# Kernel optimization log

Measured on AMD Instinct MI355X. Metric: run time of the kernel, lower is better.

Reference implementation:

```python
import jax, jax.numpy as jnp
import numpy as np

DIM, HEADS, WS, SHIFT = 192, 6, 8, 4
HEAD_DIM = DIM // HEADS
SCALE = HEAD_DIM ** -0.5
EPS = 1e-5


def _rel_pos_index(ws):
    coords = np.stack(np.meshgrid(np.arange(ws), np.arange(ws), indexing='ij'))  # [2,ws,ws]
    flat = coords.reshape(2, -1)
    rel = flat[:, :, None] - flat[:, None, :]          # [2,N,N]
    rel = rel.transpose(1, 2, 0)
    rel[:, :, 0] += ws - 1
    rel[:, :, 1] += ws - 1
    rel[:, :, 0] *= 2 * ws - 1
    return rel.sum(-1)                                  # [N,N] int


def _attn_mask(H, W, ws, shift):
    if shift == 0:
        return None
    img = np.zeros((H, W), dtype=np.float32)
    cnt = 0
    for hs in (slice(0, -ws), slice(-ws, -shift), slice(-shift, None)):
        for wsl in (slice(0, -ws), slice(-ws, -shift), slice(-shift, None)):
            img[hs, wsl] = cnt
            cnt += 1
    mw = img.reshape(H // ws, ws, W // ws, ws).transpose(0, 2, 1, 3).reshape(-1, ws * ws)  # [nW,N]
    m = mw[:, None, :] - mw[:, :, None]
    return jnp.asarray(np.where(m != 0, -100.0, 0.0).astype(np.float32))  # [nW,N,N]


def _ln(x, w, b):
    mu = x.mean(-1, keepdims=True)
    var = ((x - mu) ** 2).mean(-1, keepdims=True)
    return (x - mu) * jax.lax.rsqrt(var + EPS) * w + b


def setup_inputs() -> dict:
    key = jax.random.key(0)
    ks = jax.random.split(key, 10)
    B, H, W, C = 64, 56, 56, DIM
    hid = 4 * C
    p = lambda k, sh, s=0.02: jax.random.normal(k, sh, jnp.float32) * s
    return {
        'x': jax.random.normal(ks[0], (B, H * W, C), jnp.float32),
        'ln1_w': jnp.ones((C,), jnp.float32), 'ln1_b': jnp.zeros((C,), jnp.float32),
        'qkv_w': p(ks[1], (C, 3 * C)), 'qkv_b': jnp.zeros((3 * C,), jnp.float32),
        'proj_w': p(ks[2], (C, C)), 'proj_b': jnp.zeros((C,), jnp.float32),
        'rpb_table': p(ks[3], ((2 * WS - 1) ** 2, HEADS)),
        'ln2_w': jnp.ones((C,), jnp.float32), 'ln2_b': jnp.zeros((C,), jnp.float32),
        'fc1_w': p(ks[4], (C, hid)), 'fc1_b': jnp.zeros((hid,), jnp.float32),
        'fc2_w': p(ks[5], (hid, C)), 'fc2_b': jnp.zeros((C,), jnp.float32),
        'H': H, 'W': W,
    }


def reference(x, ln1_w, ln1_b, qkv_w, qkv_b, proj_w, proj_b, rpb_table,
              ln2_w, ln2_b, fc1_w, fc1_b, fc2_w, fc2_b, H, W):
    B, L, C = x.shape
    N = WS * WS
    shortcut = x
    xn = _ln(x, ln1_w, ln1_b).reshape(B, H, W, C)
    xn = jnp.roll(xn, (-SHIFT, -SHIFT), (1, 2))
    # window partition -> [B*nW, N, C]
    xw = xn.reshape(B, H // WS, WS, W // WS, WS, C).transpose(0, 1, 3, 2, 4, 5)
    xw = xw.reshape(-1, N, C)
    B_ = xw.shape[0]
    qkv = (xw @ qkv_w + qkv_b).reshape(B_, N, 3, HEADS, HEAD_DIM).transpose(2, 0, 3, 1, 4)
    q, k, v = qkv[0], qkv[1], qkv[2]                    # [B_,h,N,d]
    attn = jnp.einsum('bhnd,bhmd->bhnm', q * SCALE, k)
    bias = rpb_table[_rel_pos_index(WS).reshape(-1)].reshape(N, N, HEADS).transpose(2, 0, 1)
    attn = attn + bias[None]
    mask = _attn_mask(H, W, WS, SHIFT)
    if mask is not None:
        nW = mask.shape[0]
        attn = attn.reshape(B_ // nW, nW, HEADS, N, N) + mask[None, :, None]
        attn = attn.reshape(B_, HEADS, N, N)
    attn = jax.nn.softmax(attn, axis=-1)
    out = jnp.einsum('bhnm,bhmd->bhnd', attn, v).transpose(0, 2, 1, 3).reshape(B_, N, C)
    out = out @ proj_w + proj_b
    # window reverse
    out = out.reshape(B, H // WS, W // WS, WS, WS, C).transpose(0, 1, 3, 2, 4, 5).reshape(B, H, W, C)
    out = jnp.roll(out, (SHIFT, SHIFT), (1, 2))
    x = shortcut + out.reshape(B, L, C)
    h = jax.nn.gelu(_ln(x, ln2_w, ln2_b) @ fc1_w + fc1_b, approximate=False)
    return x + (h @ fc2_w + fc2_b)
```

## Files before the change

### kernel.cpp

```cpp
#include <hip/hip_runtime.h>
#include <cstdint>
#include <cstddef>

#define WS_ 8
#define DIM_ 192
#define HEADS_ 6
#define HD_ 32
#define HH_ 56
#define NW_ 7
#define NWIN_ 49
#define LTOK_ 3136
#define NTOK_ 200704
#define NWTOT_ 3136
#define SHIFT_ 4
#define SCALE_ 0.17677669529663687f

typedef unsigned short ushort_t;
typedef __attribute__((ext_vector_type(8))) short short8;
typedef __attribute__((ext_vector_type(4))) short bf16x4;
typedef __attribute__((ext_vector_type(4))) float floatx4;
typedef __attribute__((ext_vector_type(8))) unsigned short ushort8;

__device__ __forceinline__ float b2f(ushort_t u) {
    union { unsigned int i; float f; } c; c.i = ((unsigned int)u) << 16; return c.f;
}
__device__ __forceinline__ ushort_t f2b(float f) {
    union { float f; unsigned int i; } c; c.f = f;
    unsigned int u = c.i;
    unsigned int r = (u + 0x7FFFu + ((u >> 16) & 1u)) >> 16;
    return (ushort_t)r;
}

__device__ __forceinline__ void load_lds16(const void* g, void* l) {
    __builtin_amdgcn_global_load_lds(
        (const __attribute__((address_space(1))) unsigned int*)g,
        (__attribute__((address_space(3))) unsigned int*)l, 16, 0, 0);
}

__device__ __forceinline__ int win_row_to_img(int r) {
    int win = r >> 6, n = r & 63;
    int b = win / NWIN_, wI = win - b * NWIN_;
    int wh = wI / NW_, wwi = wI - wh * NW_;
    int i = n >> 3, j = n & 7;
    int hh = wh * WS_ + i + SHIFT_; if (hh >= HH_) hh -= HH_;
    int ww = wwi * WS_ + j + SHIFT_; if (ww >= HH_) ww -= HH_;
    return b * LTOK_ + hh * HH_ + ww;
}

__global__ void transpose_kernel(const float* __restrict__ in,
                                 ushort_t* __restrict__ out, int K, int N) {
    int id = blockIdx.x * 256 + threadIdx.x;
    if (id >= K * N) return;
    int k = id / N, n = id - k * N;
    out[(size_t)n * K + k] = f2b(in[id]);
}

__global__ void bias_kernel(const float* __restrict__ rpb, float* __restrict__ Spre) {
    int th = blockIdx.x;
    int type = th / HEADS_, head = th - type * HEADS_;
    for (int idx = threadIdx.x; idx < 4096; idx += 256) {
        int q = idx >> 6, k = idx & 63;
        int i1 = q >> 3, j1 = q & 7, i2 = k >> 3, j2 = k & 7;
        int rel = (i1 - i2 + 7) * 15 + (j1 - j2 + 7);
        float v = rpb[rel * HEADS_ + head];
        int rh1 = (type & 2) ? (i1 < 4 ? 1 : 2) : 0;
        int rw1 = (type & 1) ? (j1 < 4 ? 1 : 2) : 0;
        int rh2 = (type & 2) ? (i2 < 4 ? 1 : 2) : 0;
        int rw2 = (type & 1) ? (j2 < 4 ? 1 : 2) : 0;
        if (rh1 != rh2 || rw1 != rw2) v -= 100.0f;
        Spre[(size_t)th * 4096 + idx] = v;
    }
}

template <bool PERMUTE>
__global__ __launch_bounds__(256) void ln_kernel(const float* __restrict__ xin,
                                                 const float* __restrict__ w,
                                                 const float* __restrict__ bia,
                                                 ushort_t* __restrict__ out,
                                                 int rowOff) {
    int t = blockIdx.x * 4 + (threadIdx.x >> 6);
    int lane = threadIdx.x & 63;
    int src = PERMUTE ? win_row_to_img(rowOff + t) : t;
    const float* xp = xin + (size_t)src * DIM_;
    float v0 = xp[lane];
    float v1 = xp[lane + 64];
    float v2 = xp[lane + 128];
    float s = v0 + v1 + v2;
    float ss = v0 * v0 + v1 * v1 + v2 * v2;
#pragma unroll
    for (int o = 32; o > 0; o >>= 1) {
        s += __shfl_xor(s, o);
        ss += __shfl_xor(ss, o);
    }
    float mu = s * (1.0f / 192.0f);
    float var = ss * (1.0f / 192.0f) - mu * mu;
    float inv = rsqrtf(var + 1e-5f);
    ushort_t* op = out + (size_t)t * DIM_;
    op[lane]       = f2b((v0 - mu) * inv * w[lane]       + bia[lane]);
    op[lane + 64]  = f2b((v1 - mu) * inv * w[lane + 64]  + bia[lane + 64]);
    op[lane + 128] = f2b((v2 - mu) * inv * w[lane + 128] + bia[lane + 128]);
}

#define EPI_STORE 0
#define EPI_GELU 1
#define EPI_PROJ 2
#define EPI_FC2 3
#define EPI_QKV 4

template <int EPI>
__global__ __launch_bounds__(256) void gemm_kernel(const ushort_t* __restrict__ A,
                                                   const ushort_t* __restrict__ Bt,
                                                   const float* __restrict__ bias,
                                                   void* __restrict__ outv,
                                                   const float* __restrict__ aux,
                                                   int K, int N, int rowOff) {
    __shared__ char smem[40960];

    int tid = threadIdx.x;
    int wave = tid >> 6, lane = tid & 63;
    int quad = lane >> 4, l16 = lane & 15;
    int wave_r = wave >> 1, wave_c = wave & 1;
    int row0 = blockIdx.x * 128;
    int n0 = blockIdx.y * 192;

    floatx4 acc[4][6];
#pragma unroll
    for (int rt = 0; rt < 4; ++rt)
#pragma unroll
        for (int ct = 0; ct < 6; ++ct)
#pragma unroll
            for (int e = 0; e < 4; ++e) acc[rt][ct][e] = 0.0f;

    int nk = K >> 5;

    auto stage = [&](int kk, int buf) {
#pragma unroll
        for (int j = 0; j < 2; ++j) {
            int o = (tid + j * 256) * 16;
            int row = o >> 6, kb = o & 63;
            const ushort_t* g = A + (size_t)(row0 + row) * K + kk * 32 + (kb >> 1);
            load_lds16(g, smem + buf * 8192 + o);
        }
#pragma unroll
        for (int j = 0; j < 3; ++j) {
            int o = (tid + j * 256) * 16;
            int row = o >> 6, kb = o & 63;
            const ushort_t* g = Bt + (size_t)(n0 + row) * K + kk * 32 + (kb >> 1);
            load_lds16(g, smem + 16384 + buf * 12288 + o);
        }
    };

    stage(0, 0);
    for (int kk = 0; kk < nk; ++kk) {
        int cur = kk & 1;
        __syncthreads();
        if (kk + 1 < nk) stage(kk + 1, cur ^ 1);

        short8 a[4];
#pragma unroll
        for (int rt = 0; rt < 4; ++rt)
            a[rt] = *(const short8*)(smem + cur * 8192 +
                     ((wave_r * 64 + rt * 16 + l16) * 64 + quad * 16));
#pragma unroll
        for (int ct = 0; ct < 6; ++ct) {
            short8 b = *(const short8*)(smem + 16384 + cur * 12288 +
                        ((wave_c * 96 + ct * 16 + l16) * 64 + quad * 16));
#pragma unroll
            for (int rt = 0; rt < 4; ++rt)
                acc[rt][ct] = __builtin_amdgcn_mfma_f32_16x16x32_bf16(a[rt], b, acc[rt][ct], 0, 0, 0);
        }
    }

#pragma unroll
    for (int ct = 0; ct < 6; ++ct) {
        int c = n0 + wave_c * 96 + ct * 16 + l16;
        float bs = bias[c];
#pragma unroll
        for (int rt = 0; rt < 4; ++rt) {
#pragma unroll
            for (int r = 0; r < 4; ++r) {
                int rr = row0 + wave_r * 64 + rt * 16 + quad * 4 + r;
                float val = acc[rt][ct][r] + bs;
                if (EPI == EPI_STORE) {
                    ((ushort_t*)outv)[(size_t)rr * N + c] = f2b(val);
                } else if (EPI == EPI_QKV) {
                    float sv = (c < DIM_) ? val * SCALE_ : val;
                    ((ushort_t*)outv)[(size_t)rr * N + c] = f2b(sv);
                } else if (EPI == EPI_GELU) {
                    float g = 0.5f * val * (1.0f + erff(val * 0.70710678118654752f));
                    ((ushort_t*)outv)[(size_t)rr * N + c] = f2b(g);
                } else if (EPI == EPI_PROJ) {
                    int dst = win_row_to_img(rowOff + rr);
                    size_t idx = (size_t)dst * DIM_ + c;
                    ((float*)outv)[idx] = val + aux[idx];
                } else {
                    size_t idx = (size_t)rr * DIM_ + c;
                    ((float*)outv)[idx] = val + aux[idx];
                }
            }
        }
    }
}

__global__ __launch_bounds__(256) void attn_kernel(const ushort_t* __restrict__ qkv,
                                                   const float* __restrict__ Spre,
                                                   ushort_t* __restrict__ aout,
                                                   int win0, int nwh) {
    __shared__ char smem[32768];
    int wave = threadIdx.x >> 6;
    int whid = blockIdx.x * 4 + wave;
    if (whid >= nwh) return;
    int lane = threadIdx.x & 63;
    int l16 = lane & 15, quad = lane >> 4;
    int winl = whid / HEADS_, head = whid - winl * HEADS_;
    int wI = (win0 + winl) % NWIN_;
    int wh = wI / NW_, wwi = wI - wh * NW_;
    int type = ((wh == 6) ? 2 : 0) + ((wwi == 6) ? 1 : 0);

    const ushort_t* qb = qkv + (size_t)(winl * 64) * 576 + head * HD_;

    short8 vfrag[2][2];
#pragma unroll
    for (int kk = 0; kk < 2; ++kk)
#pragma unroll
        for (int dt = 0; dt < 2; ++dt)
#pragma unroll
            for (int e = 0; e < 8; ++e)
                vfrag[dt][kk][e] =
                    (short)qb[(size_t)(kk * 32 + quad * 8 + e) * 576 + 2 * DIM_ + dt * 16 + l16];

    short8 kf[4], qf[4];
#pragma unroll
    for (int t = 0; t < 4; ++t) {
        kf[t] = *(const short8*)(qb + (size_t)(t * 16 + l16) * 576 + DIM_ + quad * 8);
        qf[t] = *(const short8*)(qb + (size_t)(t * 16 + l16) * 576 + quad * 8);
    }

    const float* bp = Spre + (size_t)(type * HEADS_ + head) * 4096;
    floatx4 acc[4][4];
#pragma unroll
    for (int art = 0; art < 4; ++art)
#pragma unroll
        for (int act = 0; act < 4; ++act)
            acc[art][act] = *(const floatx4*)(bp + (act * 16 + l16) * 64 + art * 16 + quad * 4);

#pragma unroll
    for (int art = 0; art < 4; ++art)
#pragma unroll
        for (int act = 0; act < 4; ++act)
            acc[art][act] = __builtin_amdgcn_mfma_f32_16x16x32_bf16(
                kf[art], qf[act], acc[art][act], 0, 0, 0);

    char* pb = smem + wave * 8192;
    int sw = (l16 & 7) << 4;
#pragma unroll
    for (int act = 0; act < 4; ++act) {
        float m = -1e30f;
#pragma unroll
        for (int art = 0; art < 4; ++art)
#pragma unroll
            for (int r = 0; r < 4; ++r) m = fmaxf(m, acc[art][act][r]);
        m = fmaxf(m, __shfl_xor(m, 16));
        m = fmaxf(m, __shfl_xor(m, 32));
        float s = 0.0f;
#pragma unroll
        for (int art = 0; art < 4; ++art)
#pragma unroll
            for (int r = 0; r < 4; ++r) {
                float e = __expf(acc[art][act][r] - m);
                acc[art][act][r] = e;
                s += e;
            }
        s += __shfl_xor(s, 16);
        s += __shfl_xor(s, 32);
        float inv = 1.0f / s;
        int q = act * 16 + l16;
        char* rowp = pb + q * 128;
#pragma unroll
        for (int art = 0; art < 4; ++art) {
            bf16x4 pk4;
#pragma unroll
            for (int r = 0; r < 4; ++r) pk4[r] = (short)f2b(acc[art][act][r] * inv);
            *(bf16x4*)(rowp + ((art * 32 + quad * 8) ^ sw)) = pk4;
        }
    }

    floatx4 accO[4][2];
#pragma unroll
    for (int ot = 0; ot < 4; ++ot)
#pragma unroll
        for (int dt = 0; dt < 2; ++dt)
#pragma unroll
            for (int e = 0; e < 4; ++e) accO[ot][dt][e] = 0.0f;
#pragma unroll
    for (int kk = 0; kk < 2; ++kk) {
        short8 pa[4];
#pragma unroll
        for (int ot = 0; ot < 4; ++ot)
            pa[ot] = *(const short8*)(pb + (ot * 16 + l16) * 128 +
                                      ((kk * 64 + quad * 16) ^ sw));
#pragma unroll
        for (int dt = 0; dt < 2; ++dt)
#pragma unroll
            for (int ot = 0; ot < 4; ++ot)
                accO[ot][dt] = __builtin_amdgcn_mfma_f32_16x16x32_bf16(
                    pa[ot], vfrag[dt][kk], accO[ot][dt], 0, 0, 0);
    }

    ushort_t* op = aout + (size_t)(winl * 64) * DIM_ + head * HD_;
#pragma unroll
    for (int ot = 0; ot < 4; ++ot)
#pragma unroll
        for (int dt = 0; dt < 2; ++dt)
#pragma unroll
            for (int r = 0; r < 4; ++r)
                op[(size_t)(ot * 16 + quad * 4 + r) * DIM_ + dt * 16 + l16] =
                    f2b(accO[ot][dt][r]);
}

__global__ __launch_bounds__(256) void mlp_kernel(const float* __restrict__ x1,
                                                  const float* __restrict__ lnw,
                                                  const float* __restrict__ lnb,
                                                  const ushort_t* __restrict__ w1t,
                                                  const float* __restrict__ b1,
                                                  const ushort_t* __restrict__ w2t,
                                                  const float* __restrict__ b2,
                                                  float* __restrict__ out) {
    __shared__ char smem[24576 + 49152];
    char* As = smem;
    char* Hs = smem + 24576;
    int tid = threadIdx.x;
    int wave = tid >> 6, lane = tid & 63;
    int quad = lane >> 4, l16 = lane & 15;
    int row0 = blockIdx.x * 64;

    {
        float wa = lnw[lane], wb = lnw[lane + 64], wc2 = lnw[lane + 128];
        float ba = lnb[lane], bb = lnb[lane + 64], bc2 = lnb[lane + 128];
        for (int i = 0; i < 16; ++i) {
            int row = i * 4 + wave;
            const float* xp = x1 + (size_t)(row0 + row) * DIM_;
            float v0 = xp[lane], v1 = xp[lane + 64], v2 = xp[lane + 128];
            float s = v0 + v1 + v2;
            float ss = v0 * v0 + v1 * v1 + v2 * v2;
#pragma unroll
            for (int o = 32; o > 0; o >>= 1) {
                s += __shfl_xor(s, o);
                ss += __shfl_xor(ss, o);
            }
            float mu = s * (1.0f / 192.0f);
            float var = ss * (1.0f / 192.0f) - mu * mu;
            float inv = rsqrtf(var + 1e-5f);
            char* rp = As + row * 384;
            int sx = (row & 7) << 4;
            *(ushort_t*)(rp + ((lane * 2) ^ sx))         = f2b((v0 - mu) * inv * wa + ba);
            *(ushort_t*)(rp + (((lane + 64) * 2) ^ sx))  = f2b((v1 - mu) * inv * wb + bb);
            *(ushort_t*)(rp + (((lane + 128) * 2) ^ sx)) = f2b((v2 - mu) * inv * wc2 + bc2);
        }
    }
    __syncthreads();

    floatx4 acc2[4][3];
#pragma unroll
    for (int rt = 0; rt < 4; ++rt)
#pragma unroll
        for (int ct = 0; ct < 3; ++ct)
#pragma unroll
            for (int e = 0; e < 4; ++e) acc2[rt][ct][e] = 0.0f;

#pragma unroll
    for (int h = 0; h < 2; ++h) {
#pragma unroll
        for (int sub = 0; sub < 2; ++sub) {
            floatx4 acc1[4][3];
#pragma unroll
            for (int rt = 0; rt < 4; ++rt)
#pragma unroll
                for (int ct = 0; ct < 3; ++ct)
#pragma unroll
                    for (int e = 0; e < 4; ++e) acc1[rt][ct][e] = 0.0f;
#pragma unroll
            for (int kk = 0; kk < 6; ++kk) {
                short8 a[4];
#pragma unroll
                for (int rt = 0; rt < 4; ++rt) {
                    int row = rt * 16 + l16;
                    a[rt] = *(const short8*)(As + row * 384 +
                             ((kk * 64 + quad * 16) ^ ((row & 7) << 4)));
                }
#pragma unroll
                for (int ct = 0; ct < 3; ++ct) {
                    int n = h * 384 + wave * 96 + sub * 48 + ct * 16 + l16;
                    short8 bfr = *(const short8*)(w1t + (size_t)n * 192 + kk * 32 + quad * 8);
#pragma unroll
                    for (int rt = 0; rt < 4; ++rt)
                        acc1[rt][ct] = __builtin_amdgcn_mfma_f32_16x16x32_bf16(
                            a[rt], bfr, acc1[rt][ct], 0, 0, 0);
                }
            }
#pragma unroll
            for (int ct = 0; ct < 3; ++ct) {
                int colh = wave * 96 + sub * 48 + ct * 16 + l16;
                float bs = b1[h * 384 + colh];
#pragma unroll
                for (int rt = 0; rt < 4; ++rt) {
#pragma unroll
                    for (int r = 0; r < 4; ++r) {
                        int row = rt * 16 + quad * 4 + r;
                        float val = acc1[rt][ct][r] + bs;
                        float g = 0.5f * val * (1.0f + erff(val * 0.70710678118654752f));
                        *(ushort_t*)(Hs + row * 768 +
                                     ((colh * 2) ^ ((row & 7) << 4))) = f2b(g);
                    }
                }
            }
        }
        __syncthreads();
#pragma unroll
        for (int kk = 0; kk < 12; ++kk) {
            short8 a[4];
#pragma unroll
            for (int rt = 0; rt < 4; ++rt) {
                int row = rt * 16 + l16;
                a[rt] = *(const short8*)(Hs + row * 768 +
                         ((kk * 64 + quad * 16) ^ ((row & 7) << 4)));
            }
#pragma unroll
            for (int ct = 0; ct < 3; ++ct) {
                int n2 = wave * 48 + ct * 16 + l16;
                short8 bfr = *(const short8*)(w2t + (size_t)n2 * 768 +
                                              h * 384 + kk * 32 + quad * 8);
#pragma unroll
                for (int rt = 0; rt < 4; ++rt)
                    acc2[rt][ct] = __builtin_amdgcn_mfma_f32_16x16x32_bf16(
                        a[rt], bfr, acc2[rt][ct], 0, 0, 0);
            }
        }
        __syncthreads();
    }

#pragma unroll
    for (int ct = 0; ct < 3; ++ct) {
        int c = wave * 48 + ct * 16 + l16;
        float bs = b2[c];
#pragma unroll
        for (int rt = 0; rt < 4; ++rt) {
#pragma unroll
            for (int r = 0; r < 4; ++r) {
                int rr = row0 + rt * 16 + quad * 4 + r;
                size_t idx = (size_t)rr * DIM_ + c;
                out[idx] = acc2[rt][ct][r] + bs + x1[idx];
            }
        }
    }
}

extern "C" void kernel_launch(void* const* d_in, const int* in_sizes, int n_in,
                              void* d_out, int out_size, void* d_ws, size_t ws_size,
                              hipStream_t stream) {
    const float* x      = (const float*)d_in[0];
    const float* ln1_w  = (const float*)d_in[1];
    const float* ln1_b  = (const float*)d_in[2];
    const float* qkv_w  = (const float*)d_in[3];
    const float* qkv_b  = (const float*)d_in[4];
    const float* proj_w = (const float*)d_in[5];
    const float* proj_b = (const float*)d_in[6];
    const float* rpb    = (const float*)d_in[7];
    const float* ln2_w  = (const float*)d_in[8];
    const float* ln2_b  = (const float*)d_in[9];
    const float* fc1_w  = (const float*)d_in[10];
    const float* fc1_b  = (const float*)d_in[11];
    const float* fc2_w  = (const float*)d_in[12];
    const float* fc2_b  = (const float*)d_in[13];

    char* ws = (char*)d_ws;
    size_t off = 0;
    auto alloc = [&](size_t bytes) -> void* {
        void* p = ws + off;
        off += (bytes + 255) & ~(size_t)255;
        return p;
    };
    ushort_t* qkv_wt  = (ushort_t*)alloc((size_t)576 * 192 * 2);
    ushort_t* proj_wt = (ushort_t*)alloc((size_t)192 * 192 * 2);
    ushort_t* fc1_wt  = (ushort_t*)alloc((size_t)768 * 192 * 2);
    ushort_t* fc2_wt  = (ushort_t*)alloc((size_t)192 * 768 * 2);
    float*    SpreT   = (float*)alloc((size_t)4 * HEADS_ * 4096 * sizeof(float));

    float* x1 = (float*)d_out;

    size_t budget = (ws_size > off + 4096) ? (ws_size - off - 4096) : 0;
    long rows = (long)(budget / 1920);
    rows = (rows / 128) * 128;
    if (rows < 128) rows = 128;
    if (rows > NTOK_) rows = NTOK_;
    int chunkRows = (int)rows;
    int Wc = chunkRows / 64;
    if (Wc > NWTOT_) Wc = NWTOT_;

    ushort_t* bufS = (ushort_t*)alloc((size_t)chunkRows * 192 * 2);
    ushort_t* bufL = (ushort_t*)alloc((size_t)chunkRows * 768 * 2);
    (void)n_in; (void)in_sizes; (void)out_size;

    transpose_kernel<<<(192 * 576 + 255) / 256, 256, 0, stream>>>(qkv_w, qkv_wt, 192, 576);
    transpose_kernel<<<(192 * 192 + 255) / 256, 256, 0, stream>>>(proj_w, proj_wt, 192, 192);
    transpose_kernel<<<(192 * 768 + 255) / 256, 256, 0, stream>>>(fc1_w, fc1_wt, 192, 768);
    transpose_kernel<<<(768 * 192 + 255) / 256, 256, 0, stream>>>(fc2_w, fc2_wt, 768, 192);
    bias_kernel<<<4 * HEADS_, 256, 0, stream>>>(rpb, SpreT);

    for (int w0 = 0; w0 < NWTOT_; w0 += Wc) {
        int wc = NWTOT_ - w0 < Wc ? NWTOT_ - w0 : Wc;
        int rowsA = wc * 64;
        ln_kernel<true><<<rowsA / 4, 256, 0, stream>>>(x, ln1_w, ln1_b, bufS, w0 * 64);
        dim3 gq(rowsA / 128, 576 / 192);
        gemm_kernel<EPI_QKV><<<gq, 256, 0, stream>>>(bufS, qkv_wt, qkv_b, bufL, nullptr, 192, 576, 0);
        int nwh = wc * HEADS_;
        attn_kernel<<<(nwh + 3) / 4, 256, 0, stream>>>(bufL, SpreT, bufS, w0, nwh);
        dim3 gp(rowsA / 128, 1);
        gemm_kernel<EPI_PROJ><<<gp, 256, 0, stream>>>(bufS, proj_wt, proj_b, x1, x, 192, 192, w0 * 64);
    }

    mlp_kernel<<<NTOK_ / 64, 256, 0, stream>>>(x1, ln2_w, ln2_b, fc1_wt, fc1_b,
                                               fc2_wt, fc2_b, x1);
}
```

Before: 1.267 ms.

## Swizzle GEMM LDS layout, split LN2 out of MLP, restructure hidden-dim loop

Adds an XOR swizzle to the LDS tiles filled by global_load_lds in the QKV/proj GEMM so that MFMA fragment reads avoid bank conflicts. LayerNorm2 moves out of the MLP kernel into a separate chunked ln_kernel pass that writes bf16 to a workspace, and the MLP kernel then loads that tile directly into swizzled LDS. The MLP hidden dimension is now processed in six groups of 128 columns instead of two halves of 384, which cuts LDS use and may raise occupancy. The cost is extra launches and an extra bf16 round trip through global memory for the normalized activations.

Measured after the change: 1.018 ms. 1.24x faster.

```diff
diff --git a/kernel.cpp b/kernel.cpp
--- a/kernel.cpp
+++ b/kernel.cpp
@@ -35,6 +35,13 @@
     __builtin_amdgcn_global_load_lds(
         (const __attribute__((address_space(1))) unsigned int*)g,
         (__attribute__((address_space(3))) unsigned int*)l, 16, 0, 0);
+}
+
+__device__ __forceinline__ int swz_row(int o) {
+    return ((o >> 7) << 1) | (((o >> 6) ^ (o >> 8)) & 1);
+}
+__device__ __forceinline__ int swz_rd(int row, int quad) {
+    return (row << 6) ^ (quad << 4) ^ ((row & 7) << 4);
 }
 
 __device__ __forceinline__ int win_row_to_img(int r) {
@@ -137,15 +144,17 @@
 #pragma unroll
         for (int j = 0; j < 2; ++j) {
             int o = (tid + j * 256) * 16;
-            int row = o >> 6, kb = o & 63;
-            const ushort_t* g = A + (size_t)(row0 + row) * K + kk * 32 + (kb >> 1);
+            int row = swz_row(o);
+            int q = ((o >> 4) & 3) ^ (row & 3);
+            const ushort_t* g = A + (size_t)(row0 + row) * K + kk * 32 + q * 8;
             load_lds16(g, smem + buf * 8192 + o);
         }
 #pragma unroll
         for (int j = 0; j < 3; ++j) {
             int o = (tid + j * 256) * 16;
-            int row = o >> 6, kb = o & 63;
-            const ushort_t* g = Bt + (size_t)(n0 + row) * K + kk * 32 + (kb >> 1);
+            int row = swz_row(o);
+            int q = ((o >> 4) & 3) ^ (row & 3);
+            const ushort_t* g = Bt + (size_t)(n0 + row) * K + kk * 32 + q * 8;
             load_lds16(g, smem + 16384 + buf * 12288 + o);
         }
     };
@@ -158,13 +167,14 @@
 
         short8 a[4];
 #pragma unroll
-        for (int rt = 0; rt < 4; ++rt)
-            a[rt] = *(const short8*)(smem + cur * 8192 +
-                     ((wave_r * 64 + rt * 16 + l16) * 64 + quad * 16));
+        for (int rt = 0; rt < 4; ++rt) {
+            int ar = wave_r * 64 + rt * 16 + l16;
+            a[rt] = *(const short8*)(smem + cur * 8192 + swz_rd(ar, quad));
+        }
 #pragma unroll
         for (int ct = 0; ct < 6; ++ct) {
-            short8 b = *(const short8*)(smem + 16384 + cur * 12288 +
-                        ((wave_c * 96 + ct * 16 + l16) * 64 + quad * 16));
+            int br = wave_c * 96 + ct * 16 + l16;
+            short8 b = *(const short8*)(smem + 16384 + cur * 12288 + swz_rd(br, quad));
 #pragma unroll
             for (int rt = 0; rt < 4; ++rt)
                 acc[rt][ct] = __builtin_amdgcn_mfma_f32_16x16x32_bf16(a[rt], b, acc[rt][ct], 0, 0, 0);
@@ -318,15 +328,14 @@
                     f2b(accO[ot][dt][r]);
 }
 
-__global__ __launch_bounds__(256) void mlp_kernel(const float* __restrict__ x1,
-                                                  const float* __restrict__ lnw,
-                                                  const float* __restrict__ lnb,
+__global__ __launch_bounds__(256) void mlp_kernel(const ushort_t* __restrict__ xn,
+                                                  const float* __restrict__ x1r,
                                                   const ushort_t* __restrict__ w1t,
                                                   const float* __restrict__ b1,
                                                   const ushort_t* __restrict__ w2t,
                                                   const float* __restrict__ b2,
                                                   float* __restrict__ out) {
-    __shared__ char smem[24576 + 49152];
+    __shared__ char smem[40960];
     char* As = smem;
     char* Hs = smem + 24576;
     int tid = threadIdx.x;
@@ -334,106 +343,89 @@
     int quad = lane >> 4, l16 = lane & 15;
     int row0 = blockIdx.x * 64;
 
-    {
-        float wa = lnw[lane], wb = lnw[lane + 64], wc2 = lnw[lane + 128];
-        float ba = lnb[lane], bb = lnb[lane + 64], bc2 = lnb[lane + 128];
-        for (int i = 0; i < 16; ++i) {
-            int row = i * 4 + wave;
-            const float* xp = x1 + (size_t)(row0 + row) * DIM_;
-            float v0 = xp[lane], v1 = xp[lane + 64], v2 = xp[lane + 128];
-            float s = v0 + v1 + v2;
-            float ss = v0 * v0 + v1 * v1 + v2 * v2;
-#pragma unroll
-            for (int o = 32; o > 0; o >>= 1) {
-                s += __shfl_xor(s, o);
-                ss += __shfl_xor(ss, o);
-            }
-            float mu = s * (1.0f / 192.0f);
-            float var = ss * (1.0f / 192.0f) - mu * mu;
-            float inv = rsqrtf(var + 1e-5f);
-            char* rp = As + row * 384;
-            int sx = (row & 7) << 4;
-            *(ushort_t*)(rp + ((lane * 2) ^ sx))         = f2b((v0 - mu) * inv * wa + ba);
-            *(ushort_t*)(rp + (((lane + 64) * 2) ^ sx))  = f2b((v1 - mu) * inv * wb + bb);
-            *(ushort_t*)(rp + (((lane + 128) * 2) ^ sx)) = f2b((v2 - mu) * inv * wc2 + bc2);
-        }
-    }
+#pragma unroll
+    for (int j = 0; j < 6; ++j) {
+        int o = (j * 256 + tid) * 16;
+        int slab = o >> 12;
+        int os = o & 4095;
+        int row = swz_row(os);
+        int q = ((os >> 4) & 3) ^ (row & 3);
+        const ushort_t* g = xn + (size_t)(row0 + row) * DIM_ + slab * 32 + q * 8;
+        load_lds16(g, As + o);
+    }
+
+    floatx4 acc2[4][3];
+#pragma unroll
+    for (int rt = 0; rt < 4; ++rt)
+#pragma unroll
+        for (int ct = 0; ct < 3; ++ct)
+#pragma unroll
+            for (int e = 0; e < 4; ++e) acc2[rt][ct][e] = 0.0f;
+
     __syncthreads();
 
-    floatx4 acc2[4][3];
-#pragma unroll
-    for (int rt = 0; rt < 4; ++rt)
-#pragma unroll
-        for (int ct = 0; ct < 3; ++ct)
-#pragma unroll
-            for (int e = 0; e < 4; ++e) acc2[rt][ct][e] = 0.0f;
-
-#pragma unroll
-    for (int h = 0; h < 2; ++h) {
-#pragma unroll
-        for (int sub = 0; sub < 2; ++sub) {
-            floatx4 acc1[4][3];
-#pragma unroll
-            for (int rt = 0; rt < 4; ++rt)
-#pragma unroll
-                for (int ct = 0; ct < 3; ++ct)
-#pragma unroll
-                    for (int e = 0; e < 4; ++e) acc1[rt][ct][e] = 0.0f;
-#pragma unroll
-            for (int kk = 0; kk < 6; ++kk) {
-                short8 a[4];
-#pragma unroll
-                for (int rt = 0; rt < 4; ++rt) {
-                    int row = rt * 16 + l16;
-                    a[rt] = *(const short8*)(As + row * 384 +
-                             ((kk * 64 + quad * 16) ^ ((row & 7) << 4)));
+#pragma unroll 1
+    for (int g = 0; g < 6; ++g) {
+        floatx4 acc1[4][2];
+#pragma unroll
+        for (int rt = 0; rt < 4; ++rt)
+#pragma unroll
+            for (int ct = 0; ct < 2; ++ct)
+#pragma unroll
+                for (int e = 0; e < 4; ++e) acc1[rt][ct][e] = 0.0f;
+#pragma unroll
+        for (int s = 0; s < 6; ++s) {
+            short8 a[4];
+#pragma unroll
+            for (int rt = 0; rt < 4; ++rt) {
+                int ar = rt * 16 + l16;
+                a[rt] = *(const short8*)(As + s * 4096 + swz_rd(ar, quad));
+            }
+#pragma unroll
+            for (int ct = 0; ct < 2; ++ct) {
+                int n = g * 128 + wave * 32 + ct * 16 + l16;
+                short8 b = *(const short8*)(w1t + (size_t)n * 192 + s * 32 + quad * 8);
+#pragma unroll
+                for (int rt = 0; rt < 4; ++rt)
+                    acc1[rt][ct] = __builtin_amdgcn_mfma_f32_16x16x32_bf16(
+                        a[rt], b, acc1[rt][ct], 0, 0, 0);
+            }
+        }
+#pragma unroll
+        for (int ct = 0; ct < 2; ++ct) {
+            int cl = wave * 32 + ct * 16 + l16;
+            float bs = b1[g * 128 + cl];
+            int kq = (cl & 31) >> 3;
+            int kb = (cl & 7) * 2;
+#pragma unroll
+            for (int rt = 0; rt < 4; ++rt) {
+#pragma unroll
+                for (int r = 0; r < 4; ++r) {
+                    int R = rt * 16 + quad * 4 + r;
+                    float val = acc1[rt][ct][r] + bs;
+                    float gg = 0.5f * val * (1.0f + erff(val * 0.70710678118654752f));
+                    *(ushort_t*)(Hs + wave * 4096 + swz_rd(R, kq) + kb) = f2b(gg);
                 }
-#pragma unroll
-                for (int ct = 0; ct < 3; ++ct) {
-                    int n = h * 384 + wave * 96 + sub * 48 + ct * 16 + l16;
-                    short8 bfr = *(const short8*)(w1t + (size_t)n * 192 + kk * 32 + quad * 8);
-#pragma unroll
-                    for (int rt = 0; rt < 4; ++rt)
-                        acc1[rt][ct] = __builtin_amdgcn_mfma_f32_16x16x32_bf16(
-                            a[rt], bfr, acc1[rt][ct], 0, 0, 0);
-                }
-            }
-#pragma unroll
-            for (int ct = 0; ct < 3; ++ct) {
-                int colh = wave * 96 + sub * 48 + ct * 16 + l16;
-                float bs = b1[h * 384 + colh];
-#pragma unroll
-                for (int rt = 0; rt < 4; ++rt) {
-#pragma unroll
-                    for (int r = 0; r < 4; ++r) {
-                        int row = rt * 16 + quad * 4 + r;
-                        float val = acc1[rt][ct][r] + bs;
-                        float g = 0.5f * val * (1.0f + erff(val * 0.70710678118654752f));
-                        *(ushort_t*)(Hs + row * 768 +
-                                     ((colh * 2) ^ ((row & 7) << 4))) = f2b(g);
-                    }
-                }
             }
         }
         __syncthreads();
 #pragma unroll
-        for (int kk = 0; kk < 12; ++kk) {
-            short8 a[4];
+        for (int s2 = 0; s2 < 4; ++s2) {
+            short8 a2[4];
 #pragma unroll
             for (int rt = 0; rt < 4; ++rt) {
-                int row = rt * 16 + l16;
-                a[rt] = *(const short8*)(Hs + row * 768 +
-                         ((kk * 64 + quad * 16) ^ ((row & 7) << 4)));
+                int ar = rt * 16 + l16;
+                a2[rt] = *(const short8*)(Hs + s2 * 4096 + swz_rd(ar, quad));
             }
 #pragma unroll
             for (int ct = 0; ct < 3; ++ct) {
                 int n2 = wave * 48 + ct * 16 + l16;
-                short8 bfr = *(const short8*)(w2t + (size_t)n2 * 768 +
-                                              h * 384 + kk * 32 + quad * 8);
+                short8 b2v = *(const short8*)(w2t + (size_t)n2 * 768 +
+                                              g * 128 + s2 * 32 + quad * 8);
 #pragma unroll
                 for (int rt = 0; rt < 4; ++rt)
                     acc2[rt][ct] = __builtin_amdgcn_mfma_f32_16x16x32_bf16(
-                        a[rt], bfr, acc2[rt][ct], 0, 0, 0);
+                        a2[rt], b2v, acc2[rt][ct], 0, 0, 0);
             }
         }
         __syncthreads();
@@ -449,7 +441,7 @@
             for (int r = 0; r < 4; ++r) {
                 int rr = row0 + rt * 16 + quad * 4 + r;
                 size_t idx = (size_t)rr * DIM_ + c;
-                out[idx] = acc2[rt][ct][r] + bs + x1[idx];
+                out[idx] = acc2[rt][ct][r] + bs + x1r[idx];
             }
         }
     }
@@ -519,6 +511,11 @@
         gemm_kernel<EPI_PROJ><<<gp, 256, 0, stream>>>(bufS, proj_wt, proj_b, x1, x, 192, 192, w0 * 64);
     }
 
-    mlp_kernel<<<NTOK_ / 64, 256, 0, stream>>>(x1, ln2_w, ln2_b, fc1_wt, fc1_b,
-                                               fc2_wt, fc2_b, x1);
-}
+    for (int t0 = 0; t0 < NTOK_; t0 += chunkRows) {
+        int tc = NTOK_ - t0 < chunkRows ? NTOK_ - t0 : chunkRows;
+        ln_kernel<false><<<tc / 4, 256, 0, stream>>>(x1 + (size_t)t0 * 192, ln2_w, ln2_b, bufS, 0);
+        mlp_kernel<<<tc / 64, 256, 0, stream>>>(bufS, x1 + (size_t)t0 * 192,
+                                                fc1_wt, fc1_b, fc2_wt, fc2_b,
+                                                x1 + (size_t)t0 * 192);
+    }
+}
```
